# Optimization experiments

Hardware: AMD Instinct MI355X
Metric: run time of the kernel (lower is better)

The kernel has to match this reference:

```python
import jax, jax.numpy as jnp
import numpy as np

B, S, D, H = 2, 2048, 1024, 16
HD = D // H  # head_dim = 64


def setup_inputs() -> dict:
    key = jax.random.key(0)
    ks = jax.random.split(key, 8)
    scale = 0.02
    return {
        "hidden_states": jax.random.normal(ks[0], (B, S, D), dtype=jnp.float32),
        "attn_mask": jnp.zeros((B, 1, 1, S), dtype=jnp.float32),  # additive mask
        "Wq": jax.random.normal(ks[1], (D, D), dtype=jnp.float32) * scale,
        "bq": jnp.zeros((D,), dtype=jnp.float32),
        "Wk": jax.random.normal(ks[2], (D, D), dtype=jnp.float32) * scale,
        "bk": jnp.zeros((D,), dtype=jnp.float32),
        "Wv": jax.random.normal(ks[3], (D, D), dtype=jnp.float32) * scale,
        "bv": jnp.zeros((D,), dtype=jnp.float32),
    }


def reference(hidden_states, attn_mask, Wq, bq, Wk, bk, Wv, bv):
    # QKV projections: nn.Linear(dim, dim) -> x @ W.T + b
    def proj(x, W, b):
        y = jnp.einsum("bsd,ed->bse", x, W) + b
        # split heads: [B, S, D] -> [B, H, S, HD]
        return y.reshape(B, S, H, HD).transpose(0, 2, 1, 3)

    q = proj(hidden_states, Wq, bq)
    k = proj(hidden_states, Wk, bk)
    v = proj(hidden_states, Wv, bv)

    # scaled dot-product scores + additive mask (hack_torch_trace(scores, mask))
    scores = jnp.einsum("bhqd,bhkd->bhqk", q, k) / jnp.sqrt(jnp.float32(HD))
    scores = scores + attn_mask  # broadcast [B,1,1,S]
    probs = jax.nn.softmax(scores, axis=-1)  # attn dropout = identity (eval)

    ctx = jnp.einsum("bhqk,bhkd->bhqd", probs, v)
    # merge heads: [B, H, S, HD] -> [B, S, D]
    attn_outputs = ctx.transpose(0, 2, 1, 3).reshape(B, S, D)
    return attn_outputs
```

## Files before the change

### kernel.cpp

```cpp
#include <hip/hip_runtime.h>
#include <hip/hip_bf16.h>
#include <math.h>


typedef __bf16 bf16_t;
typedef __attribute__((ext_vector_type(8))) __bf16 bf16x8;
typedef __attribute__((ext_vector_type(4))) __bf16 bf16x4;
typedef __attribute__((ext_vector_type(4))) float f32x4;

#define B_  2
#define S_  2048
#define D_  1024
#define H_  16
#define HD_ 64
#define M_  (B_ * S_)
#define K_  D_
#define NT_ (S_ / 64)
#define LOG2E 1.44269504f
#define CS_Q (0.125f * LOG2E)

#if __has_builtin(__builtin_amdgcn_exp2f)
#define EXP2F(x) __builtin_amdgcn_exp2f(x)
#else
#define EXP2F(x) exp2f(x)
#endif

__device__ __forceinline__ f32x4 mfma16x16x32(bf16x8 a, bf16x8 b, f32x4 c) {
    return __builtin_amdgcn_mfma_f32_16x16x32_bf16(a, b, c, 0, 0, 0);
}

__device__ __forceinline__ void gload_lds16(const bf16_t* g, bf16_t* l) {
    __builtin_amdgcn_global_load_lds(
        (const __attribute__((address_space(1))) void*)g,
        (__attribute__((address_space(3))) void*)l,
        16, 0, 0);
}

__global__ void cvt_all(const float* __restrict__ hs, const float* __restrict__ wq,
                        const float* __restrict__ wk, const float* __restrict__ wv,
                        const float* __restrict__ mask,
                        bf16_t* __restrict__ Xb, bf16_t* __restrict__ Wb3,
                        float* __restrict__ wfp, bf16_t* __restrict__ wfb) {
    const int i = blockIdx.x * blockDim.x + threadIdx.x;
    if (i >= 1835008) {
        const int off = i - 1835008;
        if (off < 1024) {
            float4 v = ((const float4*)mask)[off];
            float4 w4;
            w4.x = exp2f(v.x * LOG2E); w4.y = exp2f(v.y * LOG2E);
            w4.z = exp2f(v.z * LOG2E); w4.w = exp2f(v.w * LOG2E);
            ((float4*)wfp)[off] = w4;
            const int k4 = off * 4;
            const int bb = k4 >> 11, k = k4 & 2047;
            const int t  = k >> 6,  kt = k & 63;
            const int nb = kt >> 4, kgf = (kt >> 2) & 3;
            bf16x4 wb4;
            wb4[0] = (bf16_t)w4.x; wb4[1] = (bf16_t)w4.y;
            wb4[2] = (bf16_t)w4.z; wb4[3] = (bf16_t)w4.w;
            *(bf16x4*)&wfb[(((size_t)bb * 32 + t) * 4 + kgf) * 16 + nb * 4] = wb4;
        }
        return;
    }
    const float* src; bf16_t* dst; int off;
    if (i < 1048576)      { src = hs; dst = Xb;            off = i; }
    else if (i < 1310720) { src = wq; dst = Wb3;           off = i - 1048576; }
    else if (i < 1572864) { src = wk; dst = Wb3 + 1048576; off = i - 1310720; }
    else                  { src = wv; dst = Wb3 + 2097152; off = i - 1572864; }
    float4 v = ((const float4*)src)[off];
    bf16x4 o;
    o[0] = (bf16_t)v.x; o[1] = (bf16_t)v.y;
    o[2] = (bf16_t)v.z; o[3] = (bf16_t)v.w;
    ((bf16x4*)dst)[off] = o;
}

__global__ __launch_bounds__(256, 2)
void gemm_qkv(const bf16_t* __restrict__ Xb, const bf16_t* __restrict__ Wb3,
              const float* __restrict__ bq, const float* __restrict__ bk,
              const float* __restrict__ bv,
              const float* __restrict__ wfp,
              bf16_t* __restrict__ Qo, bf16_t* __restrict__ Ko,
              bf16_t* __restrict__ Vf) {
    __shared__ bf16_t smem[2][8192];
    const int z = blockIdx.z;
    const bf16_t* Wb = Wb3 + (size_t)z * (D_ * K_);
    const float* bias = (z == 0) ? bq : (z == 1) ? bk : bv;

    const int tid  = threadIdx.x;
    const int lane = tid & 63;
    const int w    = tid >> 6;
    const int wr   = w >> 1, wc = w & 1;
    const int m0   = blockIdx.y * 128;
    const int n0   = blockIdx.x * 128;

    f32x4 acc[4][4];
    const f32x4 fzero = {0.f, 0.f, 0.f, 0.f};
#pragma unroll
    for (int i = 0; i < 4; i++)
#pragma unroll
        for (int j = 0; j < 4; j++) acc[i][j] = fzero;

    const int koff = (lane >> 4) * 8;

    auto stage = [&](int k0, int buf) {
#pragma unroll
        for (int i = 0; i < 4; i++) {
            const int chunk  = w * 4 + i;
            const int byteoff = chunk * 1024 + lane * 16;
            bf16_t* ldst = &smem[buf][chunk * 512];
            const bf16_t* gsrc;
            if (byteoff < 8192) {
                int row = byteoff >> 6;
                int col = (byteoff & 63) >> 1;
                gsrc = Xb + (size_t)(m0 + row) * K_ + k0 + col;
            } else {
                int bo  = byteoff - 8192;
                int row = bo >> 6;
                int col = (bo & 63) >> 1;
                gsrc = Wb + (size_t)(n0 + row) * K_ + k0 + col;
            }
            gload_lds16(gsrc, ldst);
        }
    };

    stage(0, 0);
    __syncthreads();

    for (int kk = 0; kk < K_ / 32; ++kk) {
        const int cur = kk & 1;
        if (kk + 1 < K_ / 32) stage((kk + 1) * 32, cur ^ 1);

        bf16x8 af[4], bfr[4];
#pragma unroll
        for (int m = 0; m < 4; m++) {
            int row = wr * 64 + m * 16 + (lane & 15);
            af[m] = *(const bf16x8*)&smem[cur][row * 32 + koff];
        }
#pragma unroll
        for (int n = 0; n < 4; n++) {
            int row = wc * 64 + n * 16 + (lane & 15);
            bfr[n] = *(const bf16x8*)&smem[cur][4096 + row * 32 + koff];
        }
#pragma unroll
        for (int m = 0; m < 4; m++)
#pragma unroll
            for (int n = 0; n < 4; n++)
                acc[m][n] = mfma16x16x32(af[m], bfr[n], acc[m][n]);

        __syncthreads();
    }

#pragma unroll
    for (int m = 0; m < 4; m++) {
        const int gm    = m0 + wr * 64 + m * 16 + ((lane >> 4) << 2);
        const int bidx  = gm >> 11;
        const int sbase = gm & 2047;
#pragma unroll
        for (int n = 0; n < 4; n++) {
            const int gn = n0 + wc * 64 + n * 16 + (lane & 15);
            const int h  = gn >> 6, hd = gn & 63;
            const float bias_v = bias[gn];
            const size_t bh = (size_t)bidx * H_ + h;
            if (z == 2) {
                const int t   = sbase >> 6, k0i = sbase & 63;
                const int nb  = k0i >> 4, kgf = (k0i >> 2) & 3;
                const int db  = hd >> 4,  lqf = hd & 15;
                const float4 w4 = *(const float4*)&wfp[bidx * S_ + sbase];
                bf16x4 pack;
                pack[0] = (bf16_t)((acc[m][n][0] + bias_v) * w4.x);
                pack[1] = (bf16_t)((acc[m][n][1] + bias_v) * w4.y);
                pack[2] = (bf16_t)((acc[m][n][2] + bias_v) * w4.z);
                pack[3] = (bf16_t)((acc[m][n][3] + bias_v) * w4.w);
                bf16_t* dst = Vf + ((bh * 32 + t) * 4 + db) * 1024 +
                    (kgf * 16 + lqf) * 16 + nb * 4;
                *(bf16x4*)dst = pack;
            } else if (z == 0) {
#pragma unroll
                for (int j = 0; j < 4; j++) {
                    float y = (acc[m][n][j] + bias_v) * CS_Q;
                    Qo[(bh * S_ + sbase + j) * HD_ + hd] = (bf16_t)y;
                }
            } else {
#pragma unroll
                for (int j = 0; j < 4; j++) {
                    float y = acc[m][n][j] + bias_v;
                    Ko[(bh * S_ + sbase + j) * HD_ + hd] = (bf16_t)y;
                }
            }
        }
    }
}

__global__ __launch_bounds__(256, 2)
void attn_fwd(const bf16_t* __restrict__ Qb, const bf16_t* __restrict__ Kb,
              const bf16_t* __restrict__ Vf, const bf16_t* __restrict__ Wfb,
              float* __restrict__ out) {
    const int flat = blockIdx.x;
    const int xcd  = flat & 7;
    const int idx  = flat >> 3;
    const int bh   = xcd * 4 + (idx >> 4);
    const int qt   = idx & 15;
    const int b    = bh >> 4;
    const int h    = bh & 15;

    const int tid  = threadIdx.x, lane = tid & 63, w = tid >> 6;

    const bf16_t* Qh = Qb + (size_t)bh * S_ * HD_;
    const bf16_t* Kh = Kb + (size_t)bh * S_ * HD_;
    const bf16_t* Vh = Vf + (size_t)bh * 32 * 4096;
    const bf16_t* Wh = Wfb + (size_t)b * 32 * 64;

    __shared__ char ShBuf[16384];

    const int lq   = lane & 15;
    const int kg   = lane >> 4;
    const int koff = kg * 8;
    const int rsub = lane >> 3;
    const int csl8 = (lane & 7) * 8;

    auto stageK = [&](int kv0, int buf) {
        bf16_t* base = (bf16_t*)(ShBuf + buf * 8192);
#pragma unroll
        for (int i = 0; i < 2; i++) {
            const int c = w * 2 + i;
            bf16_t* ldst = base + c * 512;
            const int cel = csl8 ^ (rsub * 8);
            const bf16_t* gsrc = Kh + (size_t)(kv0 + c * 8 + rsub) * HD_ + cel;
            gload_lds16(gsrc, ldst);
        }
    };

    const int qbase = qt * 128 + w * 32;
    bf16x8 qf0[2], qf1[2];
#pragma unroll
    for (int s = 0; s < 2; s++) {
        const bf16_t* qr = Qh + (size_t)(qbase + s * 16 + lq) * HD_;
        qf0[s] = *(const bf16x8*)(qr + koff);
        qf1[s] = *(const bf16x8*)(qr + 32 + koff);
    }

    const f32x4 fzero = {0.f, 0.f, 0.f, 0.f};
    f32x4 of[2][4];
    f32x4 of_l[2];
#pragma unroll
    for (int s = 0; s < 2; s++) {
        of_l[s] = fzero;
#pragma unroll
        for (int i = 0; i < 4; i++) of[s][i] = fzero;
    }

    const int rdsw = (lq & 7) << 4;

    bf16x8 va[4], vb[4], wf0, wf1;
    {
        const bf16_t* Vt_ = Vh;
#pragma unroll
        for (int db = 0; db < 4; db++) {
            const bf16_t* vp = Vt_ + db * 1024 + lane * 16;
            va[db] = *(const bf16x8*)(vp);
            vb[db] = *(const bf16x8*)(vp + 8);
        }
        wf0 = *(const bf16x8*)(Wh + kg * 16);
        wf1 = *(const bf16x8*)(Wh + kg * 16 + 8);
    }
    stageK(0, 0);
    __syncthreads();

    for (int t = 0; t < NT_; ++t) {
        const int cur = t & 1;

        bf16x8 nva[4], nvb[4], nwf0, nwf1;
        if (t + 1 < NT_) {
            const bf16_t* Vn = Vh + (size_t)(t + 1) * 4096;
#pragma unroll
            for (int db = 0; db < 4; db++) {
                const bf16_t* vp = Vn + db * 1024 + lane * 16;
                nva[db] = *(const bf16x8*)(vp);
                nvb[db] = *(const bf16x8*)(vp + 8);
            }
            const bf16_t* wp = Wh + (size_t)(t + 1) * 64 + kg * 16;
            nwf0 = *(const bf16x8*)(wp);
            nwf1 = *(const bf16x8*)(wp + 8);
            stageK((t + 1) * 64, cur ^ 1);
        }

        const char* KB = ShBuf + cur * 8192;

        bf16x8 kf0[4], kf1[4];
#pragma unroll
        for (int nb = 0; nb < 4; nb++) {
            const char* kr = KB + (nb * 16 + lq) * 128;
            kf0[nb] = *(const bf16x8*)(kr + ((kg * 16) ^ rdsw));
            kf1[nb] = *(const bf16x8*)(kr + ((64 + kg * 16) ^ rdsw));
        }

#pragma unroll
        for (int s = 0; s < 2; s++) {
            f32x4 sc[4];
#pragma unroll
            for (int nb = 0; nb < 4; nb++) {
                f32x4 tacc = fzero;
                tacc = mfma16x16x32(kf0[nb], qf0[s], tacc);
                tacc = mfma16x16x32(kf1[nb], qf1[s], tacc);
                sc[nb] = tacc;
            }

            bf16x8 pa0, pa1;
#pragma unroll
            for (int nb = 0; nb < 4; nb++)
#pragma unroll
                for (int j = 0; j < 4; j++) {
                    float p = EXP2F(sc[nb][j]);
                    const int e = (nb & 1) * 4 + j;
                    if (nb < 2) pa0[e] = (bf16_t)p; else pa1[e] = (bf16_t)p;
                }

#pragma unroll
            for (int db = 0; db < 4; db++) {
                of[s][db] = mfma16x16x32(pa0, va[db], of[s][db]);
                of[s][db] = mfma16x16x32(pa1, vb[db], of[s][db]);
            }
            of_l[s] = mfma16x16x32(pa0, wf0, of_l[s]);
            of_l[s] = mfma16x16x32(pa1, wf1, of_l[s]);
        }

        __syncthreads();

        if (t + 1 < NT_) {
#pragma unroll
            for (int db = 0; db < 4; db++) { va[db] = nva[db]; vb[db] = nvb[db]; }
            wf0 = nwf0; wf1 = nwf1;
        }
    }

#pragma unroll
    for (int s = 0; s < 2; s++) {
        float inv[4];
#pragma unroll
        for (int j = 0; j < 4; j++) inv[j] = 1.0f / of_l[s][j];
#pragma unroll
        for (int db = 0; db < 4; db++) {
            const int d = h * HD_ + db * 16 + lq;
#pragma unroll
            for (int j = 0; j < 4; j++) {
                const int row = qbase + s * 16 + kg * 4 + j;
                out[((size_t)b * S_ + row) * D_ + d] = of[s][db][j] * inv[j];
            }
        }
    }
}

extern "C" void kernel_launch(void* const* d_in, const int* in_sizes, int n_in,
                              void* d_out, int out_size, void* d_ws, size_t ws_size,
                              hipStream_t stream) {
    const float* hs   = (const float*)d_in[0];
    const float* mask = (const float*)d_in[1];
    const float* Wq   = (const float*)d_in[2];
    const float* bq   = (const float*)d_in[3];
    const float* Wk   = (const float*)d_in[4];
    const float* bk   = (const float*)d_in[5];
    const float* Wv   = (const float*)d_in[6];
    const float* bv   = (const float*)d_in[7];
    float* out = (float*)d_out;

    char* ws = (char*)d_ws;
    bf16_t* Xb  = (bf16_t*)(ws);
    bf16_t* Wb3 = (bf16_t*)(ws + 8388608);
    bf16_t* Qb  = (bf16_t*)(ws + 14680064);
    bf16_t* Kb  = (bf16_t*)(ws + 23068672);
    bf16_t* Vfr = (bf16_t*)(ws + 31457280);
    float*  wfp = (float*)(ws + 39845888);
    bf16_t* wfb = (bf16_t*)(ws + 39862272);

    cvt_all<<<7172, 256, 0, stream>>>(hs, Wq, Wk, Wv, mask, Xb, Wb3, wfp, wfb);

    dim3 ggrid(D_ / 128, M_ / 128, 3);
    gemm_qkv<<<ggrid, 256, 0, stream>>>(Xb, Wb3, bq, bk, bv, wfp, Qb, Kb, Vfr);

    attn_fwd<<<512, 256, 0, stream>>>(Qb, Kb, Vfr, wfb, out);
}
```

Baseline: 87.59 us.

## Split attention KV loop across two warp groups and merge partial sums in LDS

Doubles the attention block to 512 threads, with two halves of warps each processing half of the key/value tiles for the same query rows (split-K over the sequence). Each half has its own double-buffered K staging area. At the end the second half writes its unnormalized output and row sums to shared memory, and the first half adds them and normalizes. This aims to raise parallelism and latency hiding in the serial KV loop, at the cost of more LDS, register pressure under the larger launch bound, and an extra reduction pass. The merge works without rescaling because the kernel uses no running max.

```diff
diff --git a/kernel.cpp b/kernel.cpp
--- a/kernel.cpp
+++ b/kernel.cpp
@@ -16,6 +16,7 @@
 #define M_  (B_ * S_)
 #define K_  D_
 #define NT_ (S_ / 64)
+#define NTH_ (NT_ / 2)
 #define LOG2E 1.44269504f
 #define CS_Q (0.125f * LOG2E)
 
@@ -190,7 +191,7 @@
     }
 }
 
-__global__ __launch_bounds__(256, 2)
+__global__ __launch_bounds__(512, 4)
 void attn_fwd(const bf16_t* __restrict__ Qb, const bf16_t* __restrict__ Kb,
               const bf16_t* __restrict__ Vf, const bf16_t* __restrict__ Wfb,
               float* __restrict__ out) {
@@ -203,13 +204,17 @@
     const int h    = bh & 15;
 
     const int tid  = threadIdx.x, lane = tid & 63, w = tid >> 6;
+    const int wq   = w & 3;
+    const int half = w >> 2;
 
     const bf16_t* Qh = Qb + (size_t)bh * S_ * HD_;
     const bf16_t* Kh = Kb + (size_t)bh * S_ * HD_;
     const bf16_t* Vh = Vf + (size_t)bh * 32 * 4096;
     const bf16_t* Wh = Wfb + (size_t)b * 32 * 64;
 
-    __shared__ char ShBuf[16384];
+    __shared__ char ShBuf[33280];
+    float* exf = (float*)ShBuf;
+    float* exl = (float*)(ShBuf + 32768);
 
     const int lq   = lane & 15;
     const int kg   = lane >> 4;
@@ -218,10 +223,10 @@
     const int csl8 = (lane & 7) * 8;
 
     auto stageK = [&](int kv0, int buf) {
-        bf16_t* base = (bf16_t*)(ShBuf + buf * 8192);
+        bf16_t* base = (bf16_t*)(ShBuf + (half * 2 + buf) * 8192);
 #pragma unroll
         for (int i = 0; i < 2; i++) {
-            const int c = w * 2 + i;
+            const int c = wq * 2 + i;
             bf16_t* ldst = base + c * 512;
             const int cel = csl8 ^ (rsub * 8);
             const bf16_t* gsrc = Kh + (size_t)(kv0 + c * 8 + rsub) * HD_ + cel;
@@ -229,7 +234,7 @@
         }
     };
 
-    const int qbase = qt * 128 + w * 32;
+    const int qbase = qt * 128 + wq * 32;
     bf16x8 qf0[2], qf1[2];
 #pragma unroll
     for (int s = 0; s < 2; s++) {
@@ -249,27 +254,30 @@
     }
 
     const int rdsw = (lq & 7) << 4;
+    const int t0 = half * NTH_;
 
     bf16x8 va[4], vb[4], wf0, wf1;
     {
-        const bf16_t* Vt_ = Vh;
+        const bf16_t* Vt_ = Vh + (size_t)t0 * 4096;
 #pragma unroll
         for (int db = 0; db < 4; db++) {
             const bf16_t* vp = Vt_ + db * 1024 + lane * 16;
             va[db] = *(const bf16x8*)(vp);
             vb[db] = *(const bf16x8*)(vp + 8);
         }
-        wf0 = *(const bf16x8*)(Wh + kg * 16);
-        wf1 = *(const bf16x8*)(Wh + kg * 16 + 8);
-    }
-    stageK(0, 0);
+        const bf16_t* wp = Wh + (size_t)t0 * 64 + kg * 16;
+        wf0 = *(const bf16x8*)(wp);
+        wf1 = *(const bf16x8*)(wp + 8);
+    }
+    stageK(t0 * 64, 0);
     __syncthreads();
 
-    for (int t = 0; t < NT_; ++t) {
-        const int cur = t & 1;
+    for (int tt = 0; tt < NTH_; ++tt) {
+        const int t   = t0 + tt;
+        const int cur = tt & 1;
 
         bf16x8 nva[4], nvb[4], nwf0, nwf1;
-        if (t + 1 < NT_) {
+        if (tt + 1 < NTH_) {
             const bf16_t* Vn = Vh + (size_t)(t + 1) * 4096;
 #pragma unroll
             for (int db = 0; db < 4; db++) {
@@ -283,7 +291,7 @@
             stageK((t + 1) * 64, cur ^ 1);
         }
 
-        const char* KB = ShBuf + cur * 8192;
+        const char* KB = ShBuf + (half * 2 + cur) * 8192;
 
         bf16x8 kf0[4], kf1[4];
 #pragma unroll
@@ -325,25 +333,57 @@
 
         __syncthreads();
 
-        if (t + 1 < NT_) {
+        if (tt + 1 < NTH_) {
 #pragma unroll
             for (int db = 0; db < 4; db++) { va[db] = nva[db]; vb[db] = nvb[db]; }
             wf0 = nwf0; wf1 = nwf1;
         }
     }
 
-#pragma unroll
-    for (int s = 0; s < 2; s++) {
-        float inv[4];
-#pragma unroll
-        for (int j = 0; j < 4; j++) inv[j] = 1.0f / of_l[s][j];
-#pragma unroll
-        for (int db = 0; db < 4; db++) {
-            const int d = h * HD_ + db * 16 + lq;
-#pragma unroll
-            for (int j = 0; j < 4; j++) {
-                const int row = qbase + s * 16 + kg * 4 + j;
-                out[((size_t)b * S_ + row) * D_ + d] = of[s][db][j] * inv[j];
+    const int thr = wq * 64 + lane;
+    if (half == 1) {
+#pragma unroll
+        for (int s = 0; s < 2; s++)
+#pragma unroll
+            for (int db = 0; db < 4; db++)
+#pragma unroll
+                for (int j = 0; j < 4; j++)
+                    exf[(s * 16 + db * 4 + j) * 256 + thr] = of[s][db][j];
+        if (lq == 0) {
+#pragma unroll
+            for (int s = 0; s < 2; s++)
+#pragma unroll
+                for (int j = 0; j < 4; j++)
+                    exl[((wq * 4 + kg) * 2 + s) * 4 + j] = of_l[s][j];
+        }
+    }
+    __syncthreads();
+    if (half == 0) {
+#pragma unroll
+        for (int s = 0; s < 2; s++) {
+#pragma unroll
+            for (int db = 0; db < 4; db++)
+#pragma unroll
+                for (int j = 0; j < 4; j++)
+                    of[s][db][j] += exf[(s * 16 + db * 4 + j) * 256 + thr];
+#pragma unroll
+            for (int j = 0; j < 4; j++)
+                of_l[s][j] += exl[((wq * 4 + kg) * 2 + s) * 4 + j];
+        }
+
+#pragma unroll
+        for (int s = 0; s < 2; s++) {
+            float inv[4];
+#pragma unroll
+            for (int j = 0; j < 4; j++) inv[j] = 1.0f / of_l[s][j];
+#pragma unroll
+            for (int db = 0; db < 4; db++) {
+                const int d = h * HD_ + db * 16 + lq;
+#pragma unroll
+                for (int j = 0; j < 4; j++) {
+                    const int row = qbase + s * 16 + kg * 4 + j;
+                    out[((size_t)b * S_ + row) * D_ + d] = of[s][db][j] * inv[j];
+                }
             }
         }
     }
@@ -376,5 +416,5 @@
     dim3 ggrid(D_ / 128, M_ / 128, 3);
     gemm_qkv<<<ggrid, 256, 0, stream>>>(Xb, Wb3, bq, bk, bv, wfp, Qb, Kb, Vfr);
 
-    attn_fwd<<<512, 256, 0, stream>>>(Qb, Kb, Vfr, wfb, out);
-}
+    attn_fwd<<<512, 512, 0, stream>>>(Qb, Kb, Vfr, wfb, out);
+}
```

After: 120.9 us. +38.0%, slower.
